# Kernel tuning notes

Measured on AMD Instinct MI355X. Metric: run time of the kernel, lower is better.

Reference implementation:

```python
import jax, jax.numpy as jnp
import numpy as np

C = 256        # channels per FPN level (in_channels == representation_size)
PATCH = 5      # GNN kernel_size == stride
NEG_SLOPE = 0.2
K = 7          # node_connectivities[0]


def _conv1x1(x, w, b):
    return jnp.einsum('bchw,oc->bohw', x, w) + b[None, :, None, None]


def _conv3x3(x, w, b):
    y = jax.lax.conv_general_dilated(x, w, (1, 1), 'SAME',
                                     dimension_numbers=('NCHW', 'OIHW', 'NCHW'))
    return y + b[None, :, None, None]


def _nearest(x, hout, wout):
    hin, win = x.shape[-2:]
    ih = (jnp.arange(hout) * hin) // hout
    iw = (jnp.arange(wout) * win) // wout
    return x[..., ih, :][..., iw]


def _topk_edges(score, k, n):
    # torch: A.scatter(1, topk_idx, topk_val); edge = nonzero(triu(A)); edge=[col,row]
    vals, idx = jax.lax.top_k(score, k)          # per-row top-k
    row = jnp.repeat(jnp.arange(n), k)
    col = idx.reshape(-1)
    val = vals.reshape(-1)
    # triu keeps col>=row; GATv2Conv removes self loops then re-adds one per node
    mask = (col > row) & (val != 0.0)
    loop = jnp.arange(n)
    src = jnp.concatenate([col, loop])           # PyG edge_index[0] = source
    dst = jnp.concatenate([row, loop])
    emask = jnp.concatenate([mask, jnp.ones((n,), bool)])
    return src, dst, emask


def _gatv2(x, src, dst, emask, wl, bl, wr, br, att, bias, n):
    heads, dout = att.shape
    xl = (x @ wl + bl).reshape(n, heads, dout)   # source transform (lin_l)
    xr = (x @ wr + br).reshape(n, heads, dout)   # target transform (lin_r)
    m = xl[src] + xr[dst]                        # [E, H, D]
    e = jnp.sum(jax.nn.leaky_relu(m, NEG_SLOPE) * att[None], axis=-1)  # [E, H]
    e = jnp.where(emask[:, None], e, -1e30)
    emax = jax.ops.segment_max(e, dst, num_segments=n)
    w = jnp.exp(e - emax[dst]) * emask[:, None]
    denom = jax.ops.segment_sum(w, dst, num_segments=n)
    alpha = w / (denom[dst] + 1e-16)
    out = jax.ops.segment_sum(alpha[..., None] * xl[src], dst, num_segments=n)
    return out.reshape(n, heads * dout) + bias


def _gnn(x, p, k):
    # x: [1, C, H, W], H,W divisible by PATCH
    _, c, hh, ww = x.shape
    nh, nw = hh // PATCH, ww // PATCH
    n = nh * nw
    patches = x[0].reshape(c, nh, PATCH, nw, PATCH).transpose(1, 3, 0, 2, 4)
    patches = patches.reshape(n, c, PATCH, PATCH)
    emb = jax.nn.relu(jnp.einsum('ncij,ocij->no', patches, p['conv1_w']) + p['conv1_b'])
    emb = jax.nn.relu(emb @ p['fc2_w'].T + p['fc2_b'])
    # feature-similarity kNN graph
    src, dst, em = _topk_edges(emb @ emb.T, k, n)
    h = jax.nn.elu(_gatv2(emb, src, dst, em, *p['g1'], n))
    h = jax.nn.elu(_gatv2(h, src, dst, em, *p['g2'], n))
    # spatial kNN graph (k smallest distances; self distance 0 drops out via val!=0)
    ii, jj = jnp.meshgrid(jnp.arange(nh) * PATCH, jnp.arange(nw) * PATCH, indexing='ij')
    centers = jnp.stack([ii.reshape(-1), jj.reshape(-1)], -1).astype(x.dtype)
    dist = jnp.sqrt(jnp.sum((centers[:, None] - centers[None]) ** 2, -1))
    src2, dst2, em2 = _topk_edges(-dist, k, n)
    h2 = jax.nn.elu(_gatv2(emb, src2, dst2, em2, *p['g3'], n))
    h2 = jax.nn.elu(_gatv2(h2, src2, dst2, em2, *p['g4'], n))
    hc = jax.nn.relu(jnp.concatenate([h, h2], 1) @ p['fc3_w'].T + p['fc3_b']) + h2
    # torch: reshape(dim,dim,C).swapdims(-1,0) -> [C, nw, nh]
    grid = jnp.transpose(hc.reshape(nh, nw, c), (2, 1, 0))
    # ConvTranspose2d(C, C, 5, stride=5): non-overlapping tiling
    up = jnp.einsum('cij,coab->oiajb', grid, p['convT_w'])
    up = up.reshape(c, nw * PATCH, nh * PATCH) + p['convT_b'][:, None, None]
    return jax.nn.relu(up)[None]


def _forward(feat0, feat1, inner_w, inner_b, layer_w, layer_b, convT_w, convT_b,
             conv1_w, conv1_b, fc2_w, fc2_b, fc3_w, fc3_b,
             g1_wl, g1_bl, g1_wr, g1_br, g1_att, g1_bias,
             g2_wl, g2_bl, g2_wr, g2_br, g2_att, g2_bias,
             g3_wl, g3_bl, g3_wr, g3_br, g3_att, g3_bias,
             g4_wl, g4_bl, g4_wr, g4_br, g4_att, g4_bias, k):
    feats = [feat0, feat1]
    xs = []
    for i, f in enumerate(feats):
        p = dict(conv1_w=conv1_w[i], conv1_b=conv1_b[i],
                 fc2_w=fc2_w[i], fc2_b=fc2_b[i],
                 fc3_w=fc3_w[i], fc3_b=fc3_b[i],
                 convT_w=convT_w[i], convT_b=convT_b[i],
                 g1=(g1_wl[i], g1_bl[i], g1_wr[i], g1_br[i], g1_att[i], g1_bias[i]),
                 g2=(g2_wl[i], g2_bl[i], g2_wr[i], g2_br[i], g2_att[i], g2_bias[i]),
                 g3=(g3_wl[i], g3_bl[i], g3_wr[i], g3_br[i], g3_att[i], g3_bias[i]),
                 g4=(g4_wl[i], g4_bl[i], g4_wr[i], g4_br[i], g4_att[i], g4_bias[i]))
        xs.append(f + _gnn(f, p, k))
    # top-down FPN
    last = _conv1x1(xs[1], inner_w[1], inner_b[1])
    out1 = _conv3x3(last, layer_w[1], layer_b[1])
    inner0 = _conv1x1(xs[0], inner_w[0], inner_b[0])
    td = _nearest(last, xs[0].shape[-2], xs[0].shape[-1])
    out0 = _conv3x3(inner0 + td, layer_w[0], layer_b[0])
    return out0, out1


def setup_inputs() -> dict:
    key = jax.random.key(0)
    keys = jax.random.split(key, 48)
    it = iter(range(48))
    def rn(shape, s=0.05):
        return (jax.random.normal(keys[next(it)], shape) * s).astype(jnp.float32)
    H8 = 8 * C
    inp = dict(
        feat0=rn((1, C, 200, 200), 1.0),
        feat1=rn((1, C, 100, 100), 1.0),
        inner_w=rn((2, C, C)), inner_b=rn((2, C)),
        layer_w=rn((2, C, C, 3, 3)), layer_b=rn((2, C)),
        convT_w=rn((2, C, C, PATCH, PATCH)), convT_b=rn((2, C)),
        conv1_w=rn((2, C, C, PATCH, PATCH)), conv1_b=rn((2, C)),
        fc2_w=rn((2, C, C)), fc2_b=rn((2, C)),
        fc3_w=rn((2, C, 2 * C)), fc3_b=rn((2, C)),
        g1_wl=rn((2, C, H8)), g1_bl=rn((2, H8)), g1_wr=rn((2, C, H8)), g1_br=rn((2, H8)),
        g1_att=rn((2, 8, C)), g1_bias=rn((2, H8)),
        g2_wl=rn((2, H8, C)), g2_bl=rn((2, C)), g2_wr=rn((2, H8, C)), g2_br=rn((2, C)),
        g2_att=rn((2, 1, C)), g2_bias=rn((2, C)),
        g3_wl=rn((2, C, H8)), g3_bl=rn((2, H8)), g3_wr=rn((2, C, H8)), g3_br=rn((2, H8)),
        g3_att=rn((2, 8, C)), g3_bias=rn((2, H8)),
        g4_wl=rn((2, H8, C)), g4_bl=rn((2, C)), g4_wr=rn((2, H8, C)), g4_br=rn((2, C)),
        g4_att=rn((2, 1, C)), g4_bias=rn((2, C)),
        k=K,
    )
    return inp


def reference(feat0, feat1, inner_w, inner_b, layer_w, layer_b, convT_w, convT_b,
              conv1_w, conv1_b, fc2_w, fc2_b, fc3_w, fc3_b,
              g1_wl, g1_bl, g1_wr, g1_br, g1_att, g1_bias,
              g2_wl, g2_bl, g2_wr, g2_br, g2_att, g2_bias,
              g3_wl, g3_bl, g3_wr, g3_br, g3_att, g3_bias,
              g4_wl, g4_bl, g4_wr, g4_br, g4_att, g4_bias, k):
    return _forward(feat0, feat1, inner_w, inner_b, layer_w, layer_b, convT_w, convT_b,
                    conv1_w, conv1_b, fc2_w, fc2_b, fc3_w, fc3_b,
                    g1_wl, g1_bl, g1_wr, g1_br, g1_att, g1_bias,
                    g2_wl, g2_bl, g2_wr, g2_br, g2_att, g2_bias,
                    g3_wl, g3_bl, g3_wr, g3_br, g3_att, g3_bias,
                    g4_wl, g4_bl, g4_wr, g4_br, g4_att, g4_bias, k)
```

## Files before the change

### kernel.cpp

```cpp
#include <hip/hip_runtime.h>
#include <cstdint>
#include <cstddef>
#include <math.h>

#define KNN 7

using short8  = __attribute__((ext_vector_type(8))) short;
using floatx4 = __attribute__((ext_vector_type(4))) float;

static const size_t OFF_ARENA = 0;
static const size_t OFF_XS0   = 10240000;
static const size_t OFF_XS1   = 20480000;
static const size_t OFF_LAST  = 23040000;
static const size_t OFF_EMB   = 25600000;
static const size_t OFF_EMB2  = 26009600;
static const size_t OFF_XL    = 26419200;
static const size_t OFF_H1    = 32972800;
static const size_t OFF_XL2   = 36249600;
static const size_t OFF_CAT   = 37068800;
static const size_t OFF_HC    = 37888000;
static const size_t OFF_SRCF  = 38400000;
static const size_t OFF_SRCS  = 38411200;
static const size_t OFF_BF_A  = 38422400;
static const size_t OFF_BF_W  = 40122400;

static __device__ __forceinline__ unsigned short f2bf(float f) {
    union { float f; unsigned u; } v; v.f = f;
    unsigned u = v.u;
    unsigned r = u + 0x7fffu + ((u >> 16) & 1u);
    return (unsigned short)(r >> 16);
}

static __device__ __forceinline__ void glds16(const void* g, void* l) {
    __builtin_amdgcn_global_load_lds((const __attribute__((address_space(1))) void*)g,
                                     (__attribute__((address_space(3))) void*)l, 16, 0, 0);
}

template<int ACT, bool BIAS>
__global__ __launch_bounds__(256)
void gemm_k(const float* __restrict__ A, const float* __restrict__ B,
            const float* __restrict__ bias, float* __restrict__ C, int M, int N, int K)
{
    __shared__ float As[16][68];
    __shared__ float Bs[16][68];
    const int tid = threadIdx.x;
    const int bm0 = blockIdx.y * 64;
    const int bn0 = blockIdx.x * 64;
    const int tx = tid & 15, ty = tid >> 4;
    const int lrow = tid >> 2;
    const int lk4  = (tid & 3) << 2;
    const int m = bm0 + lrow;
    const int nn = bn0 + lrow;
    const bool aok = m < M, bok = nn < N;
    float acc[4][4] = {{0.f,0.f,0.f,0.f},{0.f,0.f,0.f,0.f},{0.f,0.f,0.f,0.f},{0.f,0.f,0.f,0.f}};

    float4 va = {0.f,0.f,0.f,0.f}, vb = {0.f,0.f,0.f,0.f};
    if (aok) va = *(const float4*)(A + (size_t)m * K + lk4);
    if (bok) vb = *(const float4*)(B + (size_t)nn * K + lk4);

    for (int k0 = 0; k0 < K; k0 += 16) {
        As[lk4+0][lrow]=va.x; As[lk4+1][lrow]=va.y; As[lk4+2][lrow]=va.z; As[lk4+3][lrow]=va.w;
        Bs[lk4+0][lrow]=vb.x; Bs[lk4+1][lrow]=vb.y; Bs[lk4+2][lrow]=vb.z; Bs[lk4+3][lrow]=vb.w;
        __syncthreads();
        float4 na = {0.f,0.f,0.f,0.f}, nb = {0.f,0.f,0.f,0.f};
        const bool more = (k0 + 16) < K;
        if (more) {
            if (aok) na = *(const float4*)(A + (size_t)m * K + (k0 + 16 + lk4));
            if (bok) nb = *(const float4*)(B + (size_t)nn * K + (k0 + 16 + lk4));
        }
        #pragma unroll
        for (int k = 0; k < 16; k++) {
            const float4 av = *(const float4*)&As[k][ty << 2];
            const float4 bv = *(const float4*)&Bs[k][tx << 2];
            const float a0=av.x,a1=av.y,a2=av.z,a3=av.w;
            const float b0=bv.x,b1=bv.y,b2=bv.z,b3=bv.w;
            acc[0][0]=fmaf(a0,b0,acc[0][0]); acc[0][1]=fmaf(a0,b1,acc[0][1]);
            acc[0][2]=fmaf(a0,b2,acc[0][2]); acc[0][3]=fmaf(a0,b3,acc[0][3]);
            acc[1][0]=fmaf(a1,b0,acc[1][0]); acc[1][1]=fmaf(a1,b1,acc[1][1]);
            acc[1][2]=fmaf(a1,b2,acc[1][2]); acc[1][3]=fmaf(a1,b3,acc[1][3]);
            acc[2][0]=fmaf(a2,b0,acc[2][0]); acc[2][1]=fmaf(a2,b1,acc[2][1]);
            acc[2][2]=fmaf(a2,b2,acc[2][2]); acc[2][3]=fmaf(a2,b3,acc[2][3]);
            acc[3][0]=fmaf(a3,b0,acc[3][0]); acc[3][1]=fmaf(a3,b1,acc[3][1]);
            acc[3][2]=fmaf(a3,b2,acc[3][2]); acc[3][3]=fmaf(a3,b3,acc[3][3]);
        }
        __syncthreads();
        va = na; vb = nb;
    }
    #pragma unroll
    for (int i = 0; i < 4; i++) {
        const int mm = bm0 + (ty << 2) + i;
        if (mm >= M) continue;
        #pragma unroll
        for (int jj = 0; jj < 4; jj++) {
            const int nc = bn0 + (tx << 2) + jj;
            if (nc >= N) continue;
            float v = acc[i][jj];
            if (BIAS) v += bias[nc];
            if (ACT == 1) v = fmaxf(v, 0.f);
            C[(size_t)mm * N + nc] = v;
        }
    }
}

template<int ACT, bool BIAS>
static inline void gemm32(hipStream_t s, const float* A, const float* B, const float* bias,
                          float* C, int M, int N, int K)
{
    dim3 g((N + 63) / 64, (M + 63) / 64);
    gemm_k<ACT, BIAS><<<g, dim3(256), 0, s>>>(A, B, bias, C, M, N, K);
}

__global__ __launch_bounds__(256)
void gemm32_sk_k(const float* __restrict__ A, const float* __restrict__ B,
                 float* __restrict__ part, int M, int N, int K, int Kc)
{
    __shared__ float As[16][68];
    __shared__ float Bs[16][68];
    const int tid = threadIdx.x;
    const int bm0 = blockIdx.y * 64;
    const int bn0 = blockIdx.x * 64;
    const int sblk = blockIdx.z;
    const int kbeg = sblk * Kc;
    const int kend = (kbeg + Kc < K) ? kbeg + Kc : K;
    const int tx = tid & 15, ty = tid >> 4;
    const int lrow = tid >> 2;
    const int lk4  = (tid & 3) << 2;
    const int m = bm0 + lrow;
    const int nn = bn0 + lrow;
    const bool aok = m < M, bok = nn < N;
    float acc[4][4] = {{0.f,0.f,0.f,0.f},{0.f,0.f,0.f,0.f},{0.f,0.f,0.f,0.f},{0.f,0.f,0.f,0.f}};

    float4 va = {0.f,0.f,0.f,0.f}, vb = {0.f,0.f,0.f,0.f};
    if (aok) va = *(const float4*)(A + (size_t)m * K + kbeg + lk4);
    if (bok) vb = *(const float4*)(B + (size_t)nn * K + kbeg + lk4);

    for (int k0 = kbeg; k0 < kend; k0 += 16) {
        As[lk4+0][lrow]=va.x; As[lk4+1][lrow]=va.y; As[lk4+2][lrow]=va.z; As[lk4+3][lrow]=va.w;
        Bs[lk4+0][lrow]=vb.x; Bs[lk4+1][lrow]=vb.y; Bs[lk4+2][lrow]=vb.z; Bs[lk4+3][lrow]=vb.w;
        __syncthreads();
        float4 na = {0.f,0.f,0.f,0.f}, nb = {0.f,0.f,0.f,0.f};
        const bool more = (k0 + 16) < kend;
        if (more) {
            if (aok) na = *(const float4*)(A + (size_t)m * K + (k0 + 16 + lk4));
            if (bok) nb = *(const float4*)(B + (size_t)nn * K + (k0 + 16 + lk4));
        }
        #pragma unroll
        for (int k = 0; k < 16; k++) {
            const float4 av = *(const float4*)&As[k][ty << 2];
            const float4 bv = *(const float4*)&Bs[k][tx << 2];
            const float a0=av.x,a1=av.y,a2=av.z,a3=av.w;
            const float b0=bv.x,b1=bv.y,b2=bv.z,b3=bv.w;
            acc[0][0]=fmaf(a0,b0,acc[0][0]); acc[0][1]=fmaf(a0,b1,acc[0][1]);
            acc[0][2]=fmaf(a0,b2,acc[0][2]); acc[0][3]=fmaf(a0,b3,acc[0][3]);
            acc[1][0]=fmaf(a1,b0,acc[1][0]); acc[1][1]=fmaf(a1,b1,acc[1][1]);
            acc[1][2]=fmaf(a1,b2,acc[1][2]); acc[1][3]=fmaf(a1,b3,acc[1][3]);
            acc[2][0]=fmaf(a2,b0,acc[2][0]); acc[2][1]=fmaf(a2,b1,acc[2][1]);
            acc[2][2]=fmaf(a2,b2,acc[2][2]); acc[2][3]=fmaf(a2,b3,acc[2][3]);
            acc[3][0]=fmaf(a3,b0,acc[3][0]); acc[3][1]=fmaf(a3,b1,acc[3][1]);
            acc[3][2]=fmaf(a3,b2,acc[3][2]); acc[3][3]=fmaf(a3,b3,acc[3][3]);
        }
        __syncthreads();
        va = na; vb = nb;
    }
    float* P = part + (size_t)sblk * M * N;
    #pragma unroll
    for (int i = 0; i < 4; i++) {
        const int mm = bm0 + (ty << 2) + i;
        if (mm >= M) continue;
        #pragma unroll
        for (int jj = 0; jj < 4; jj++) {
            const int nc = bn0 + (tx << 2) + jj;
            if (nc >= N) continue;
            P[(size_t)mm * N + nc] = acc[i][jj];
        }
    }
}

template<int ACT, bool BIAS>
__global__ void sk_reduce_k(const float* __restrict__ part, const float* __restrict__ bias,
                            float* __restrict__ C, int MN, int N, int S)
{
    const int i4 = (blockIdx.x * 256 + threadIdx.x) * 4;
    if (i4 >= MN) return;
    float4 a = *(const float4*)(part + i4);
    for (int s = 1; s < S; s++) {
        const float4 b = *(const float4*)(part + (size_t)s * MN + i4);
        a.x += b.x; a.y += b.y; a.z += b.z; a.w += b.w;
    }
    if (BIAS) {
        const int n = i4 % N;
        a.x += bias[n]; a.y += bias[n + 1]; a.z += bias[n + 2]; a.w += bias[n + 3];
    }
    if (ACT == 1) {
        a.x = fmaxf(a.x, 0.f); a.y = fmaxf(a.y, 0.f);
        a.z = fmaxf(a.z, 0.f); a.w = fmaxf(a.w, 0.f);
    }
    *(float4*)(C + i4) = a;
}

template<int ACT, bool BIAS>
static inline void gemm32_sk(hipStream_t s, const float* A, const float* B, const float* bias,
                             float* C, float* part, int M, int N, int K, int S)
{
    const int Kc = ((K / S + 15) / 16) * 16;
    dim3 g((N + 63) / 64, (M + 63) / 64, S);
    gemm32_sk_k<<<g, dim3(256), 0, s>>>(A, B, part, M, N, K, Kc);
    const int MN = M * N;
    sk_reduce_k<ACT, BIAS><<<dim3((MN / 4 + 255) / 256), dim3(256), 0, s>>>(part, bias, C, MN, N, S);
}

enum { BT_NT = 0, BT_CONV2 = 2 };

template<int BT, int ACT, int BAX, bool ADDMAT>
__global__ __launch_bounds__(256)
void bgemm_k(const unsigned short* __restrict__ A, const unsigned short* __restrict__ B,
             const float* __restrict__ bias, const float* __restrict__ bias2, int nsplit,
             const float* __restrict__ Dmat, int Dld,
             float* __restrict__ C, int M, int N, int K, int imH, int imW)
{
    __shared__ unsigned short As[3][4096];
    __shared__ unsigned short Bs[3][4096];
    const int tid  = threadIdx.x;
    const int lane = tid & 63;
    const int wid  = tid >> 6;
    const int quad = lane >> 4;
    const int l15  = lane & 15;
    const int wy = wid >> 1, wx = wid & 1;

    int bxx = blockIdx.x, byy = blockIdx.y;
    if (gridDim.y == 2) {
        const int nbx = gridDim.x;
        const int nwg = nbx * 2;
        const int hw  = byy * nbx + bxx;
        const int q = nwg >> 3, r = nwg & 7;
        const int x8 = hw & 7, d = hw >> 3;
        const int lg = (x8 < r) ? x8 * (q + 1) + d : r * (q + 1) + (x8 - r) * q + d;
        byy = lg & 1; bxx = lg >> 1;
    }
    const int bm0 = byy * 128;
    const int bn0 = bxx * 128;

    floatx4 zero = {0.f, 0.f, 0.f, 0.f};
    floatx4 acc[4][4];
    #pragma unroll
    for (int i = 0; i < 4; i++)
        #pragma unroll
        for (int j = 0; j < 4; j++) acc[i][j] = zero;

    const int l4 = lane >> 2;
    const int swc = (((lane & 3) ^ ((lane >> 3) & 3)) << 3);
    const int r0 = wid * 32 + l4;
    const int r1 = r0 + 16;
    int am0 = bm0 + r0; if (am0 > M - 1) am0 = M - 1;
    int am1 = bm0 + r1; if (am1 > M - 1) am1 = M - 1;
    const unsigned short* aP0 = A + (size_t)am0 * K + swc;
    const unsigned short* aP1 = A + (size_t)am1 * K + swc;

    const unsigned short* bP0;
    const unsigned short* bP1;
    if (BT == BT_NT) {
        int bn0r = bn0 + r0; if (bn0r > N - 1) bn0r = N - 1;
        int bn1r = bn0 + r1; if (bn1r > N - 1) bn1r = N - 1;
        bP0 = B + (size_t)bn0r * K + swc;
        bP1 = B + (size_t)bn1r * K + swc;
    } else {
        const int W2 = imW + 2;
        int pp0 = bn0 + r0; if (pp0 > N - 1) pp0 = N - 1;
        int pp1 = bn0 + r1; if (pp1 > N - 1) pp1 = N - 1;
        const int py0 = pp0 / imW, px0 = pp0 - py0 * imW;
        const int py1 = pp1 / imW, px1 = pp1 - py1 * imW;
        bP0 = B + ((size_t)(py0 + 1) * W2 + px0 + 1) * 256 + swc;
        bP1 = B + ((size_t)(py1 + 1) * W2 + px1 + 1) * 256 + swc;
    }

    auto stage = [&](int buf, int t) {
        const int k0 = t << 5;
        glds16(aP0 + k0, &As[buf][wid * 1024]);
        glds16(aP1 + k0, &As[buf][wid * 1024 + 512]);
        if (BT == BT_NT) {
            glds16(bP0 + k0, &Bs[buf][wid * 1024]);
            glds16(bP1 + k0, &Bs[buf][wid * 1024 + 512]);
        } else {
            const int jj = k0 >> 8;
            const int j3 = jj / 3;
            const ptrdiff_t toff = (ptrdiff_t)((j3 - 1) * (imW + 2) + (jj - j3 * 3 - 1)) * 256
                                 + (k0 & 255);
            glds16(bP0 + toff, &Bs[buf][wid * 1024]);
            glds16(bP1 + toff, &Bs[buf][wid * 1024 + 512]);
        }
    };
    const int rsw = ((quad ^ ((l15 >> 1) & 3)) << 3);
    auto compute = [&](int buf) {
        short8 af[4], bfr[4];
        #pragma unroll
        for (int i = 0; i < 4; i++)
            af[i] = *(const short8*)&As[buf][(wy * 64 + i * 16 + l15) * 32 + rsw];
        #pragma unroll
        for (int j = 0; j < 4; j++)
            bfr[j] = *(const short8*)&Bs[buf][(wx * 64 + j * 16 + l15) * 32 + rsw];
        #pragma unroll
        for (int i = 0; i < 4; i++)
            #pragma unroll
            for (int j = 0; j < 4; j++)
                acc[i][j] = __builtin_amdgcn_mfma_f32_16x16x32_bf16(af[i], bfr[j], acc[i][j], 0, 0, 0);
    };

    const int T = K >> 5;
    stage(0, 0);
    if (T > 1) stage(1, 1);
    int cb = 0, sb = 2;
    for (int t = 0; t < T; t++) {
        if (t < T - 1) asm volatile("s_waitcnt vmcnt(4) lgkmcnt(0)" ::: "memory");
        else           asm volatile("s_waitcnt vmcnt(0) lgkmcnt(0)" ::: "memory");
        __builtin_amdgcn_s_barrier();
        __builtin_amdgcn_sched_barrier(0);
        if (t + 2 < T) stage(sb, t + 2);
        compute(cb);
        cb = (cb == 2) ? 0 : cb + 1;
        sb = (sb == 2) ? 0 : sb + 1;
    }

    #pragma unroll
    for (int i = 0; i < 4; i++) {
        #pragma unroll
        for (int r = 0; r < 4; r++) {
            const int m = bm0 + wy * 64 + i * 16 + quad * 4 + r;
            if (m >= M) continue;
            #pragma unroll
            for (int j = 0; j < 4; j++) {
                const int n = bn0 + wx * 64 + j * 16 + l15;
                if (n >= N) continue;
                float v = acc[i][j][r];
                if (bias != nullptr)
                    v += (BAX == 0) ? bias[m] : (n < nsplit ? bias[n] : bias2[n - nsplit]);
                if (ACT == 1) v = fmaxf(v, 0.f);
                if (ADDMAT) v += Dmat[(size_t)m * Dld + n];
                C[(size_t)m * N + n] = v;
            }
        }
    }
}

template<int BT, int ACT, int BAX, bool ADDMAT>
static inline void bgemm(hipStream_t s, const unsigned short* A, const unsigned short* B,
                         const float* bias, const float* bias2, int nsplit,
                         const float* D, int Dld, float* C,
                         int M, int N, int K, int imH = 0, int imW = 0)
{
    dim3 g((N + 127) / 128, (M + 127) / 128);
    bgemm_k<BT, ACT, BAX, ADDMAT><<<g, dim3(256), 0, s>>>(A, B, bias, bias2, nsplit,
                                                          D, Dld, C, M, N, K, imH, imW);
}

__global__ __launch_bounds__(256)
void bgemm_sk_k(const unsigned short* __restrict__ A, const unsigned short* __restrict__ B,
                float* __restrict__ part, int M, int N, int K, int Kc)
{
    __shared__ unsigned short As[3][4096];
    __shared__ unsigned short Bs[3][4096];
    const int tid  = threadIdx.x;
    const int lane = tid & 63;
    const int wid  = tid >> 6;
    const int quad = lane >> 4;
    const int l15  = lane & 15;
    const int wy = wid >> 1, wx = wid & 1;
    const int bm0 = blockIdx.y * 128;
    const int bn0 = blockIdx.x * 128;
    const int kbeg = blockIdx.z * Kc;
    const int kend = (kbeg + Kc < K) ? kbeg + Kc : K;

    floatx4 zero = {0.f, 0.f, 0.f, 0.f};
    floatx4 acc[4][4];
    #pragma unroll
    for (int i = 0; i < 4; i++)
        #pragma unroll
        for (int j = 0; j < 4; j++) acc[i][j] = zero;

    const int l4 = lane >> 2;
    const int swc = (((lane & 3) ^ ((lane >> 3) & 3)) << 3);
    const int r0 = wid * 32 + l4;
    const int r1 = r0 + 16;
    int am0 = bm0 + r0; if (am0 > M - 1) am0 = M - 1;
    int am1 = bm0 + r1; if (am1 > M - 1) am1 = M - 1;
    int bn0r = bn0 + r0; if (bn0r > N - 1) bn0r = N - 1;
    int bn1r = bn0 + r1; if (bn1r > N - 1) bn1r = N - 1;
    const unsigned short* aP0 = A + (size_t)am0 * K + kbeg + swc;
    const unsigned short* aP1 = A + (size_t)am1 * K + kbeg + swc;
    const unsigned short* bP0 = B + (size_t)bn0r * K + kbeg + swc;
    const unsigned short* bP1 = B + (size_t)bn1r * K + kbeg + swc;

    auto stage = [&](int buf, int t) {
        const int k0 = t << 5;
        glds16(aP0 + k0, &As[buf][wid * 1024]);
        glds16(aP1 + k0, &As[buf][wid * 1024 + 512]);
        glds16(bP0 + k0, &Bs[buf][wid * 1024]);
        glds16(bP1 + k0, &Bs[buf][wid * 1024 + 512]);
    };
    const int rsw = ((quad ^ ((l15 >> 1) & 3)) << 3);
    auto compute = [&](int buf) {
        short8 af[4], bfr[4];
        #pragma unroll
        for (int i = 0; i < 4; i++)
            af[i] = *(const short8*)&As[buf][(wy * 64 + i * 16 + l15) * 32 + rsw];
        #pragma unroll
        for (int j = 0; j < 4; j++)
            bfr[j] = *(const short8*)&Bs[buf][(wx * 64 + j * 16 + l15) * 32 + rsw];
        #pragma unroll
        for (int i = 0; i < 4; i++)
            #pragma unroll
            for (int j = 0; j < 4; j++)
                acc[i][j] = __builtin_amdgcn_mfma_f32_16x16x32_bf16(af[i], bfr[j], acc[i][j], 0, 0, 0);
    };

    const int T = (kend - kbeg) >> 5;
    stage(0, 0);
    if (T > 1) stage(1, 1);
    int cb = 0, sb = 2;
    for (int t = 0; t < T; t++) {
        if (t < T - 1) asm volatile("s_waitcnt vmcnt(4) lgkmcnt(0)" ::: "memory");
        else           asm volatile("s_waitcnt vmcnt(0) lgkmcnt(0)" ::: "memory");
        __builtin_amdgcn_s_barrier();
        __builtin_amdgcn_sched_barrier(0);
        if (t + 2 < T) stage(sb, t + 2);
        compute(cb);
        cb = (cb == 2) ? 0 : cb + 1;
        sb = (sb == 2) ? 0 : sb + 1;
    }

    float* P = part + (size_t)blockIdx.z * M * N;
    #pragma unroll
    for (int i = 0; i < 4; i++) {
        #pragma unroll
        for (int r = 0; r < 4; r++) {
            const int m = bm0 + wy * 64 + i * 16 + quad * 4 + r;
            if (m >= M) continue;
            #pragma unroll
            for (int j = 0; j < 4; j++) {
                const int n = bn0 + wx * 64 + j * 16 + l15;
                if (n >= N) continue;
                P[(size_t)m * N + n] = acc[i][j][r];
            }
        }
    }
}

template<int ACT, bool ADDMAT>
__global__ void bsk_reduce_k(const float* __restrict__ part,
                             const float* __restrict__ bias, const float* __restrict__ bias2,
                             int nsplit, const float* __restrict__ Dmat, int Dld,
                             float* __restrict__ C, int MN, int N, int S)
{
    const int i4 = (blockIdx.x * 256 + threadIdx.x) * 4;
    if (i4 >= MN) return;
    float4 a = *(const float4*)(part + i4);
    for (int s = 1; s < S; s++) {
        const float4 b = *(const float4*)(part + (size_t)s * MN + i4);
        a.x += b.x; a.y += b.y; a.z += b.z; a.w += b.w;
    }
    const int n = i4 % N;
    const float* bb = (n < nsplit) ? (bias + n) : (bias2 + n - nsplit);
    a.x += bb[0]; a.y += bb[1]; a.z += bb[2]; a.w += bb[3];
    if (ACT == 1) {
        a.x = fmaxf(a.x, 0.f); a.y = fmaxf(a.y, 0.f);
        a.z = fmaxf(a.z, 0.f); a.w = fmaxf(a.w, 0.f);
    }
    if (ADDMAT) {
        const int m = i4 / N;
        const float4 d = *(const float4*)(Dmat + (size_t)m * Dld + n);
        a.x += d.x; a.y += d.y; a.z += d.z; a.w += d.w;
    }
    *(float4*)(C + i4) = a;
}

template<int ACT, bool ADDMAT>
static inline void bgemm_sk(hipStream_t s, const unsigned short* A, const unsigned short* B,
                            const float* bias, const float* bias2, int nsplit,
                            const float* D, int Dld, float* C, float* part,
                            int M, int N, int K, int S)
{
    const int Kc = ((K / S + 31) / 32) * 32;
    dim3 g((N + 127) / 128, (M + 127) / 128, S);
    bgemm_sk_k<<<g, dim3(256), 0, s>>>(A, B, part, M, N, K, Kc);
    const int MN = M * N;
    bsk_reduce_k<ACT, ADDMAT><<<dim3((MN / 4 + 255) / 256), dim3(256), 0, s>>>(
        part, bias, bias2, nsplit, D, Dld, C, MN, N, S);
}

__global__ void cast_bf16_k(const float* __restrict__ in, unsigned short* __restrict__ out, int total)
{
    const int i4 = (blockIdx.x * 256 + threadIdx.x) * 4;
    if (i4 + 4 <= total) {
        const float4 v = *(const float4*)(in + i4);
        ushort4 o;
        o.x = f2bf(v.x); o.y = f2bf(v.y); o.z = f2bf(v.z); o.w = f2bf(v.w);
        *(ushort4*)(out + i4) = o;
    } else {
        for (int i = i4; i < total; i++) out[i] = f2bf(in[i]);
    }
}

static inline void cast_bf(hipStream_t s, const float* in, unsigned short* out, int total)
{
    cast_bf16_k<<<dim3((total / 4 + 255) / 256), dim3(256), 0, s>>>(in, out, total);
}

__device__ __forceinline__ void cast_t_body(const float* __restrict__ in,
                                            unsigned short* __restrict__ out, int K, int N)
{
    __shared__ float tile[64][65];
    const int n0 = blockIdx.x * 64;
    const int k0 = blockIdx.y * 64;
    const int t = threadIdx.x;
    const int r = t >> 2;
    const int c4 = (t & 3) << 4;
    {
        const int k = k0 + r;
        if (k < K && n0 + c4 + 16 <= N) {
            const float4* p = (const float4*)(in + (size_t)k * N + n0 + c4);
            *(float4*)&tile[r][c4]      = p[0];
            *(float4*)&tile[r][c4 + 4]  = p[1];
            *(float4*)&tile[r][c4 + 8]  = p[2];
            *(float4*)&tile[r][c4 + 12] = p[3];
        } else {
            for (int i = 0; i < 16; i++)
                tile[r][c4 + i] = (k < K && n0 + c4 + i < N) ? in[(size_t)k * N + n0 + c4 + i] : 0.f;
        }
    }
    __syncthreads();
    const int n = n0 + r;
    if (n >= N) return;
    unsigned short tmp[16];
    #pragma unroll
    for (int i = 0; i < 16; i++) tmp[i] = f2bf(tile[c4 + i][r]);
    if (k0 + 64 <= K) {
        *(uint4*)(out + (size_t)n * K + k0 + c4)     = *(uint4*)&tmp[0];
        *(uint4*)(out + (size_t)n * K + k0 + c4 + 8) = *(uint4*)&tmp[8];
    } else {
        for (int i = 0; i < 16; i++)
            if (k0 + c4 + i < K) out[(size_t)n * K + k0 + c4 + i] = tmp[i];
    }
}

__global__ void cast_t_k(const float* __restrict__ in, unsigned short* __restrict__ out, int K, int N)
{
    cast_t_body(in, out, K, N);
}

__global__ void cast_t2_k(const float* __restrict__ in0, const float* __restrict__ in1,
                          unsigned short* __restrict__ out0, unsigned short* __restrict__ out1,
                          int K, int N)
{
    if (blockIdx.z == 0) cast_t_body(in0, out0, K, N);
    else                 cast_t_body(in1, out1, K, N);
}

static inline void cast_t(hipStream_t s, const float* in, unsigned short* out, int K, int N)
{
    cast_t_k<<<dim3((N + 63) / 64, (K + 63) / 64), dim3(256), 0, s>>>(in, out, K, N);
}

static inline void cast_t2(hipStream_t s, const float* in0, const float* in1,
                           unsigned short* out0, unsigned short* out1, int K, int N)
{
    cast_t2_k<<<dim3((N + 63) / 64, (K + 63) / 64, 2), dim3(256), 0, s>>>(in0, in1, out0, out1, K, N);
}

__global__ void cast_t_pad_k(const float* __restrict__ in, unsigned short* __restrict__ out,
                             int N, int imW)
{
    __shared__ float tile[64][65];
    const int n0 = blockIdx.x * 64;
    const int k0 = blockIdx.y * 64;
    const int t = threadIdx.x;
    const int r = t >> 2;
    const int c4 = (t & 3) << 4;
    {
        const int k = k0 + r;
        if (n0 + c4 + 16 <= N) {
            const float4* p = (const float4*)(in + (size_t)k * N + n0 + c4);
            *(float4*)&tile[r][c4]      = p[0];
            *(float4*)&tile[r][c4 + 4]  = p[1];
            *(float4*)&tile[r][c4 + 8]  = p[2];
            *(float4*)&tile[r][c4 + 12] = p[3];
        } else {
            for (int i = 0; i < 16; i++)
                tile[r][c4 + i] = (n0 + c4 + i < N) ? in[(size_t)k * N + n0 + c4 + i] : 0.f;
        }
    }
    __syncthreads();
    const int n = n0 + r;
    if (n >= N) return;
    const int py = n / imW, px = n - py * imW;
    unsigned short tmp[16];
    #pragma unroll
    for (int i = 0; i < 16; i++) tmp[i] = f2bf(tile[c4 + i][r]);
    unsigned short* o = out + ((size_t)(py + 1) * (imW + 2) + px + 1) * 256 + k0 + c4;
    *(uint4*)(o)     = *(uint4*)&tmp[0];
    *(uint4*)(o + 8) = *(uint4*)&tmp[8];
}

static inline void cast_t_pad(hipStream_t s, const float* in, unsigned short* out, int N, int imW)
{
    cast_t_pad_k<<<dim3((N + 63) / 64, 4), dim3(256), 0, s>>>(in, out, N, imW);
}

__global__ void zero_ring_k(unsigned short* __restrict__ out, int imH, int imW)
{
    const int W2 = imW + 2;
    const int nb = 2 * W2 + 2 * imH;
    const int idx = blockIdx.x * 256 + threadIdx.x;
    if (idx >= nb * 32) return;
    const int p = idx >> 5;
    const int c8 = (idx & 31) << 3;
    int row;
    if (p < W2)            row = p;
    else if (p < 2 * W2)   row = (imH + 1) * W2 + (p - W2);
    else { const int q = p - 2 * W2; const int y = q >> 1;
           row = (y + 1) * W2 + ((q & 1) ? (imW + 1) : 0); }
    *(uint4*)(out + (size_t)row * 256 + c8) = (uint4){0, 0, 0, 0};
}

static inline void zero_ring(hipStream_t s, unsigned short* out, int imH, int imW)
{
    const int tot = (2 * (imW + 2) + 2 * imH) * 32;
    zero_ring_k<<<dim3((tot + 255) / 256), dim3(256), 0, s>>>(out, imH, imW);
}

__global__ void reorder_w3_k(const float* __restrict__ in, unsigned short* __restrict__ out)
{
    const int idx = blockIdx.x * 256 + threadIdx.x;
    if (idx >= 589824) return;
    const int o = idx / 2304;
    const int r = idx - o * 2304;
    const int j = r >> 8;
    const int c = r & 255;
    out[idx] = f2bf(in[(size_t)o * 2304 + c * 9 + j]);
}

__global__ void extract_patches_k(const float* __restrict__ f, float* __restrict__ patches,
                                  int nw, int H, int total)
{
    int idx = blockIdx.x * 256 + threadIdx.x;
    if (idx >= total) return;
    int q = idx % 6400;
    int p = idx / 6400;
    int c = q / 25;
    int rem = q - c * 25;
    int a = rem / 5, b = rem - (rem / 5) * 5;
    int ih = p / nw, iw = p - (p / nw) * nw;
    patches[idx] = f[(size_t)c * H * H + (size_t)(ih * 5 + a) * H + (iw * 5 + b)];
}

__global__ void topk_feat_k(const float* __restrict__ score, int* __restrict__ srcCols, int n)
{
    const int r = blockIdx.x;
    const int lane = threadIdx.x;
    const float* row = score + (size_t)r * n;
    int   sel[KNN];
    float selv[KNN];
    #pragma unroll
    for (int t = 0; t < KNN; t++) {
        float best = -__builtin_huge_valf();
        int   bidx = 0x7fffffff;
        for (int c = lane; c < n; c += 64) {
            bool taken = false;
            #pragma unroll
            for (int u = 0; u < KNN; u++)
                if (u < t && sel[u] == c) taken = true;
            if (taken) continue;
            float v = row[c];
            if (v > best || (v == best && c < bidx)) { best = v; bidx = c; }
        }
        #pragma unroll
        for (int off = 32; off > 0; off >>= 1) {
            float ov = __shfl_down(best, off);
            int   oi = __shfl_down(bidx, off);
            if (ov > best || (ov == best && oi < bidx)) { best = ov; bidx = oi; }
        }
        best = __shfl(best, 0);
        bidx = __shfl(bidx, 0);
        sel[t] = bidx; selv[t] = best;
    }
    if (lane < KNN) {
        int c = -1; float v = 0.f;
        #pragma unroll
        for (int t = 0; t < KNN; t++)
            if (lane == t) { c = sel[t]; v = selv[t]; }
        srcCols[r * KNN + lane] = (c > r && v != 0.0f) ? c : -1;
    }
}

__global__ void topk_spatial_k(int* __restrict__ srcCols, int n, int nw)
{
    const int r = blockIdx.x;
    const int lane = threadIdx.x;
    const int ri = r / nw, rj = r - (r / nw) * nw;
    int sel[KNN];
    #pragma unroll
    for (int t = 0; t < KNN; t++) {
        int bkey = 0x7fffffff;
        for (int c = lane; c < n; c += 64) {
            bool taken = false;
            #pragma unroll
            for (int u = 0; u < KNN; u++)
                if (u < t && sel[u] == c) taken = true;
            if (taken) continue;
            const int ci = c / nw, cj = c - (c / nw) * nw;
            const int dy = (ri - ci) * 5, dx = (rj - cj) * 5;
            const int d2 = dy * dy + dx * dx;
            const int key = (d2 << 11) | c;
            if (key < bkey) bkey = key;
        }
        #pragma unroll
        for (int off = 32; off > 0; off >>= 1) {
            int ok = __shfl_down(bkey, off);
            if (ok < bkey) bkey = ok;
        }
        bkey = __shfl(bkey, 0);
        sel[t] = bkey & 2047;
    }
    if (lane < KNN) {
        int c = -1;
        #pragma unroll
        for (int t = 0; t < KNN; t++) if (lane == t) c = sel[t];
        srcCols[r * KNN + lane] = (c > r) ? c : -1;
    }
}

__global__ void gat_fused_k(const float* __restrict__ x, int xroff, int xstride,
                            const float* __restrict__ att,
                            const int* __restrict__ srcCols, const float* __restrict__ bias,
                            float* __restrict__ out, int n, int H, int ostride, int ooff)
{
    const int wid = (blockIdx.x * blockDim.x + threadIdx.x) >> 6;
    const int lane = threadIdx.x & 63;
    if (wid >= n * H) return;
    const int h = wid % H;
    const int r = wid / H;
    const int d0 = lane << 2;

    const float4 xrf  = *(const float4*)(x + (size_t)r * xstride + xroff + h * 256 + d0);
    const float4 attf = *(const float4*)(att + (size_t)h * 256 + d0);

    int srcs[8];
    #pragma unroll
    for (int s_ = 0; s_ < KNN; s_++) srcs[s_] = srcCols[r * KNN + s_];
    srcs[7] = r;

    float4 xlf[8];
    float  e[8];
    #pragma unroll
    for (int s_ = 0; s_ < 8; s_++) {
        const int c = srcs[s_];
        float4 v = {0.f, 0.f, 0.f, 0.f};
        if (c >= 0) v = *(const float4*)(x + (size_t)c * xstride + h * 256 + d0);
        xlf[s_] = v;
        float m, p = 0.f;
        m = v.x + xrf.x; m = (m > 0.f) ? m : 0.2f * m; p += m * attf.x;
        m = v.y + xrf.y; m = (m > 0.f) ? m : 0.2f * m; p += m * attf.y;
        m = v.z + xrf.z; m = (m > 0.f) ? m : 0.2f * m; p += m * attf.z;
        m = v.w + xrf.w; m = (m > 0.f) ? m : 0.2f * m; p += m * attf.w;
        #pragma unroll
        for (int off = 32; off > 0; off >>= 1) p += __shfl_down(p, off);
        e[s_] = __shfl(p, 0);
    }

    float mx = e[7];
    #pragma unroll
    for (int s_ = 0; s_ < KNN; s_++)
        if (srcs[s_] >= 0) mx = fmaxf(mx, e[s_]);
    float a[8], denom = 0.f;
    #pragma unroll
    for (int s_ = 0; s_ < 8; s_++) {
        a[s_] = (s_ == 7 || srcs[s_] >= 0) ? expf(e[s_] - mx) : 0.f;
        denom += a[s_];
    }
    const float inv = 1.f / (denom + 1e-16f);

    float o0 = 0.f, o1 = 0.f, o2 = 0.f, o3 = 0.f;
    #pragma unroll
    for (int s_ = 0; s_ < 8; s_++) {
        const float al = a[s_] * inv;
        o0 = fmaf(al, xlf[s_].x, o0); o1 = fmaf(al, xlf[s_].y, o1);
        o2 = fmaf(al, xlf[s_].z, o2); o3 = fmaf(al, xlf[s_].w, o3);
    }
    const float* bb = bias + (size_t)h * 256 + d0;
    o0 += bb[0]; o1 += bb[1]; o2 += bb[2]; o3 += bb[3];
    o0 = (o0 > 0.f) ? o0 : (expf(o0) - 1.f);
    o1 = (o1 > 0.f) ? o1 : (expf(o1) - 1.f);
    o2 = (o2 > 0.f) ? o2 : (expf(o2) - 1.f);
    o3 = (o3 > 0.f) ? o3 : (expf(o3) - 1.f);
    float4 res = {o0, o1, o2, o3};
    *(float4*)(out + (size_t)r * ostride + ooff + (size_t)h * 256 + d0) = res;
}

__global__ void scatter_convT_k(const float* __restrict__ f, const float* __restrict__ U,
                                const float* __restrict__ bias, float* __restrict__ xs,
                                int nw, int H, int total)
{
    int idx = blockIdx.x * 256 + threadIdx.x;
    if (idx >= total) return;
    int x = idx % H;
    int t = idx / H;
    int y = t % H;
    int o = t / H;
    int j = y / 5, a = y - j * 5;
    int i = x / 5, b = x - i * 5;
    int p = i * nw + j;
    float v = U[(size_t)p * 6400 + o * 25 + a * 5 + b] + bias[o];
    v = fmaxf(v, 0.f);
    xs[idx] = f[idx] + v;
}

__global__ void upsample_add_k(float* __restrict__ acc, const float* __restrict__ last,
                               int H, int Hs, int total)
{
    int idx = blockIdx.x * 256 + threadIdx.x;
    if (idx >= total) return;
    int x = idx % H;
    int t = idx / H;
    int y = t % H;
    int c = t / H;
    acc[idx] += last[(size_t)c * Hs * Hs + (size_t)(y >> 1) * Hs + (x >> 1)];
}

static void run_level(void* const* d_in, float* ws, int l, int H, hipStream_t s)
{
    const float* f = (const float*)d_in[l];
    const int nh = H / 5, nw = nh, n = nh * nw, HW = H * H;

    const float* convT_w = (const float*)d_in[6]  + (size_t)l * 1638400;
    const float* convT_b = (const float*)d_in[7]  + l * 256;
    const float* conv1_w = (const float*)d_in[8]  + (size_t)l * 1638400;
    const float* conv1_b = (const float*)d_in[9]  + l * 256;
    const float* fc2_w   = (const float*)d_in[10] + (size_t)l * 65536;
    const float* fc2_b   = (const float*)d_in[11] + l * 256;
    const float* fc3_w   = (const float*)d_in[12] + (size_t)l * 131072;
    const float* fc3_b   = (const float*)d_in[13] + l * 256;
    const float* g1_wl   = (const float*)d_in[14] + (size_t)l * 524288;
    const float* g1_bl   = (const float*)d_in[15] + l * 2048;
    const float* g1_wr   = (const float*)d_in[16] + (size_t)l * 524288;
    const float* g1_br   = (const float*)d_in[17] + l * 2048;
    const float* g1_att  = (const float*)d_in[18] + l * 2048;
    const float* g1_bias = (const float*)d_in[19] + l * 2048;
    const float* g2_wl   = (const float*)d_in[20] + (size_t)l * 524288;
    const float* g2_bl   = (const float*)d_in[21] + l * 256;
    const float* g2_wr   = (const float*)d_in[22] + (size_t)l * 524288;
    const float* g2_br   = (const float*)d_in[23] + l * 256;
    const float* g2_att  = (const float*)d_in[24] + l * 256;
    const float* g2_bias = (const float*)d_in[25] + l * 256;
    const float* g3_wl   = (const float*)d_in[26] + (size_t)l * 524288;
    const float* g3_bl   = (const float*)d_in[27] + l * 2048;
    const float* g3_wr   = (const float*)d_in[28] + (size_t)l * 524288;
    const float* g3_br   = (const float*)d_in[29] + l * 2048;
    const float* g3_att  = (const float*)d_in[30] + l * 2048;
    const float* g3_bias = (const float*)d_in[31] + l * 2048;
    const float* g4_wl   = (const float*)d_in[32] + (size_t)l * 524288;
    const float* g4_bl   = (const float*)d_in[33] + l * 256;
    const float* g4_wr   = (const float*)d_in[34] + (size_t)l * 524288;
    const float* g4_br   = (const float*)d_in[35] + l * 256;
    const float* g4_att  = (const float*)d_in[36] + l * 256;
    const float* g4_bias = (const float*)d_in[37] + l * 256;

    float* patches = ws + OFF_ARENA;
    float* xs    = ws + (l == 0 ? OFF_XS0 : OFF_XS1);
    float* emb   = ws + OFF_EMB;
    float* emb2  = ws + OFF_EMB2;
    float* score = ws + OFF_LAST;
    float* xlr   = ws + OFF_XL;
    float* h1    = ws + OFF_H1;
    float* xlr2  = ws + OFF_XL2;
    float* cat   = ws + OFF_CAT;
    float* hc    = ws + OFF_HC;
    int* srcF = (int*)(ws + OFF_SRCF);
    int* srcS = (int*)(ws + OFF_SRCS);
    unsigned short* ba = (unsigned short*)(ws + OFF_BF_A);
    unsigned short* bw = (unsigned short*)(ws + OFF_BF_W);
    float* part = ws + OFF_ARENA;

    { int tot = n * 6400;
      extract_patches_k<<<dim3((tot + 255) / 256), dim3(256), 0, s>>>(f, patches, nw, H, tot); }

    gemm32_sk<1, true>(s, patches, conv1_w, conv1_b, emb, xlr, n, 256, 6400, 16);
    gemm32<1, true>(s, emb, fc2_w, fc2_b, emb2, n, 256, 256);
    gemm32<0, false>(s, emb2, emb2, nullptr, score, n, n, 256);
    topk_feat_k<<<dim3(n), dim3(64), 0, s>>>(score, srcF, n);
    topk_spatial_k<<<dim3(n), dim3(64), 0, s>>>(srcS, n, nw);

    const int gatw1 = n * 8;
    const int gatw2 = n;

    cast_bf(s, emb2, ba, n * 256);
    cast_t2(s, g1_wl, g1_wr, bw, bw + 2048 * 256, 256, 2048);
    if (n >= 1024)
        bgemm<BT_NT, 0, 1, false>(s, ba, bw, g1_bl, g1_br, 2048, nullptr, 0, xlr, n, 4096, 256);
    else
        bgemm_sk<0, false>(s, ba, bw, g1_bl, g1_br, 2048, nullptr, 0, xlr, part, n, 4096, 256, 2);
    gat_fused_k<<<dim3((gatw1 + 3) / 4), dim3(256), 0, s>>>(xlr, 2048, 4096, g1_att, srcF, g1_bias, h1, n, 8, 2048, 0);

    cast_bf(s, h1, ba, n * 2048);
    cast_t2(s, g2_wl, g2_wr, bw, bw + 256 * 2048, 2048, 256);
    bgemm_sk<0, false>(s, ba, bw, g2_bl, g2_br, 256, nullptr, 0, xlr2, part, n, 512, 2048, 8);
    gat_fused_k<<<dim3((gatw2 + 3) / 4), dim3(256), 0, s>>>(xlr2, 256, 512, g2_att, srcF, g2_bias, cat, n, 1, 512, 0);

    cast_bf(s, emb2, ba, n * 256);
    cast_t2(s, g3_wl, g3_wr, bw, bw + 2048 * 256, 256, 2048);
    if (n >= 1024)
        bgemm<BT_NT, 0, 1, false>(s, ba, bw, g3_bl, g3_br, 2048, nullptr, 0, xlr, n, 4096, 256);
    else
        bgemm_sk<0, false>(s, ba, bw, g3_bl, g3_br, 2048, nullptr, 0, xlr, part, n, 4096, 256, 2);
    gat_fused_k<<<dim3((gatw1 + 3) / 4), dim3(256), 0, s>>>(xlr, 2048, 4096, g3_att, srcS, g3_bias, h1, n, 8, 2048, 0);

    cast_bf(s, h1, ba, n * 2048);
    cast_t2(s, g4_wl, g4_wr, bw, bw + 256 * 2048, 2048, 256);
    bgemm_sk<0, false>(s, ba, bw, g4_bl, g4_br, 256, nullptr, 0, xlr2, part, n, 512, 2048, 8);
    gat_fused_k<<<dim3((gatw2 + 3) / 4), dim3(256), 0, s>>>(xlr2, 256, 512, g4_att, srcS, g4_bias, cat, n, 1, 512, 256);

    cast_bf(s, cat, ba, n * 512);
    cast_bf(s, fc3_w, bw, 131072);
    bgemm_sk<1, true>(s, ba, bw, fc3_b, fc3_b, 256, cat + 256, 512, hc, part, n, 256, 512, 4);
    cast_bf(s, hc, ba, n * 256);
    cast_t(s, convT_w, bw, 256, 6400);
    bgemm<BT_NT, 0, 1, false>(s, ba, bw, nullptr, nullptr, 0, nullptr, 0, patches, n, 6400, 256);
    { int tot = 256 * HW;
      scatter_convT_k<<<dim3((tot + 255) / 256), dim3(256), 0, s>>>(f, patches, convT_b, xs, nw, H, tot); }
}

extern "C" void kernel_launch(void* const* d_in, const int* in_sizes, int n_in,
                              void* d_out, int out_size, void* d_ws, size_t ws_size,
                              hipStream_t stream)
{
    float* ws  = (float*)d_ws;
    float* out = (float*)d_out;

    run_level(d_in, ws, 0, 200, stream);
    run_level(d_in, ws, 1, 100, stream);

    const float* inner_w = (const float*)d_in[2];
    const float* inner_b = (const float*)d_in[3];
    const float* layer_w = (const float*)d_in[4];
    const float* layer_b = (const float*)d_in[5];
    float* xs0    = ws + OFF_XS0;
    float* xs1    = ws + OFF_XS1;
    float* last   = ws + OFF_LAST;
    float* inner0 = ws + OFF_ARENA;
    unsigned short* bimg = (unsigned short*)(ws + OFF_XL);
    unsigned short* bw1  = (unsigned short*)(ws + OFF_BF_W);
    unsigned short* bwc  = (unsigned short*)(ws + OFF_BF_W + 100000);

    cast_t(stream, xs1, bimg, 256, 10000);
    cast_bf(stream, inner_w + 65536, bw1, 65536);
    bgemm<BT_NT, 0, 0, false>(stream, bw1, bimg, inner_b + 256, nullptr, 0, nullptr, 0,
                              last, 256, 10000, 256);
    reorder_w3_k<<<dim3((589824 + 255) / 256), dim3(256), 0, stream>>>(layer_w + 589824, bwc);
    zero_ring(stream, bimg, 100, 100);
    cast_t_pad(stream, last, bimg, 10000, 100);
    bgemm<BT_CONV2, 0, 0, false>(stream, bwc, bimg, layer_b + 256, nullptr, 0, nullptr, 0,
                                 out + 10240000, 256, 10000, 2304, 100, 100);

    cast_t(stream, xs0, bimg, 256, 40000);
    cast_bf(stream, inner_w, bw1, 65536);
    bgemm<BT_NT, 0, 0, false>(stream, bw1, bimg, inner_b, nullptr, 0, nullptr, 0,
                              inner0, 256, 40000, 256);
    { int tot = 256 * 40000;
      upsample_add_k<<<dim3((tot + 255) / 256), dim3(256), 0, stream>>>(inner0, last, 200, 100, tot); }
    reorder_w3_k<<<dim3((589824 + 255) / 256), dim3(256), 0, stream>>>(layer_w, bwc);
    zero_ring(stream, bimg, 200, 200);
    cast_t_pad(stream, inner0, bimg, 40000, 200);
    bgemm<BT_CONV2, 0, 0, false>(stream, bwc, bimg, layer_b, nullptr, 0, nullptr, 0,
                                 out, 256, 40000, 2304, 200, 200);
}
```

Measured before the change: 1.156 ms.

## Replace fp32 split-K patch GEMM with bf16 hi/lo split MFMA GEMM

The patch-embedding GEMM (n x 6400 x 256) previously ran on an fp32 SIMT split-K kernel. It now splits the patches and conv weights into bf16 hi and lo parts and runs three MFMA products (hi*hi, lo*hi, hi*lo), with the K dimension split into slabs. The partial results are summed in the existing reduce kernel, which also adds bias and ReLU. This moves the dominant FLOPs onto the matrix cores while keeping close to fp32 accuracy, at the cost of extra cast passes, a weight split on every call, and a larger partial buffer to reduce.

New measurement: 1.116 ms. 1.04x faster.

```diff
diff --git a/kernel.cpp b/kernel.cpp
--- a/kernel.cpp
+++ b/kernel.cpp
@@ -31,6 +31,10 @@
     return (unsigned short)(r >> 16);
 }
 
+static __device__ __forceinline__ float bf2f(unsigned short h) {
+    union { unsigned u; float f; } v; v.u = ((unsigned)h) << 16; return v.f;
+}
+
 static __device__ __forceinline__ void glds16(const void* g, void* l) {
     __builtin_amdgcn_global_load_lds((const __attribute__((address_space(1))) void*)g,
                                      (__attribute__((address_space(3))) void*)l, 16, 0, 0);
@@ -108,105 +112,6 @@
 {
     dim3 g((N + 63) / 64, (M + 63) / 64);
     gemm_k<ACT, BIAS><<<g, dim3(256), 0, s>>>(A, B, bias, C, M, N, K);
-}
-
-__global__ __launch_bounds__(256)
-void gemm32_sk_k(const float* __restrict__ A, const float* __restrict__ B,
-                 float* __restrict__ part, int M, int N, int K, int Kc)
-{
-    __shared__ float As[16][68];
-    __shared__ float Bs[16][68];
-    const int tid = threadIdx.x;
-    const int bm0 = blockIdx.y * 64;
-    const int bn0 = blockIdx.x * 64;
-    const int sblk = blockIdx.z;
-    const int kbeg = sblk * Kc;
-    const int kend = (kbeg + Kc < K) ? kbeg + Kc : K;
-    const int tx = tid & 15, ty = tid >> 4;
-    const int lrow = tid >> 2;
-    const int lk4  = (tid & 3) << 2;
-    const int m = bm0 + lrow;
-    const int nn = bn0 + lrow;
-    const bool aok = m < M, bok = nn < N;
-    float acc[4][4] = {{0.f,0.f,0.f,0.f},{0.f,0.f,0.f,0.f},{0.f,0.f,0.f,0.f},{0.f,0.f,0.f,0.f}};
-
-    float4 va = {0.f,0.f,0.f,0.f}, vb = {0.f,0.f,0.f,0.f};
-    if (aok) va = *(const float4*)(A + (size_t)m * K + kbeg + lk4);
-    if (bok) vb = *(const float4*)(B + (size_t)nn * K + kbeg + lk4);
-
-    for (int k0 = kbeg; k0 < kend; k0 += 16) {
-        As[lk4+0][lrow]=va.x; As[lk4+1][lrow]=va.y; As[lk4+2][lrow]=va.z; As[lk4+3][lrow]=va.w;
-        Bs[lk4+0][lrow]=vb.x; Bs[lk4+1][lrow]=vb.y; Bs[lk4+2][lrow]=vb.z; Bs[lk4+3][lrow]=vb.w;
-        __syncthreads();
-        float4 na = {0.f,0.f,0.f,0.f}, nb = {0.f,0.f,0.f,0.f};
-        const bool more = (k0 + 16) < kend;
-        if (more) {
-            if (aok) na = *(const float4*)(A + (size_t)m * K + (k0 + 16 + lk4));
-            if (bok) nb = *(const float4*)(B + (size_t)nn * K + (k0 + 16 + lk4));
-        }
-        #pragma unroll
-        for (int k = 0; k < 16; k++) {
-            const float4 av = *(const float4*)&As[k][ty << 2];
-            const float4 bv = *(const float4*)&Bs[k][tx << 2];
-            const float a0=av.x,a1=av.y,a2=av.z,a3=av.w;
-            const float b0=bv.x,b1=bv.y,b2=bv.z,b3=bv.w;
-            acc[0][0]=fmaf(a0,b0,acc[0][0]); acc[0][1]=fmaf(a0,b1,acc[0][1]);
-            acc[0][2]=fmaf(a0,b2,acc[0][2]); acc[0][3]=fmaf(a0,b3,acc[0][3]);
-            acc[1][0]=fmaf(a1,b0,acc[1][0]); acc[1][1]=fmaf(a1,b1,acc[1][1]);
-            acc[1][2]=fmaf(a1,b2,acc[1][2]); acc[1][3]=fmaf(a1,b3,acc[1][3]);
-            acc[2][0]=fmaf(a2,b0,acc[2][0]); acc[2][1]=fmaf(a2,b1,acc[2][1]);
-            acc[2][2]=fmaf(a2,b2,acc[2][2]); acc[2][3]=fmaf(a2,b3,acc[2][3]);
-            acc[3][0]=fmaf(a3,b0,acc[3][0]); acc[3][1]=fmaf(a3,b1,acc[3][1]);
-            acc[3][2]=fmaf(a3,b2,acc[3][2]); acc[3][3]=fmaf(a3,b3,acc[3][3]);
-        }
-        __syncthreads();
-        va = na; vb = nb;
-    }
-    float* P = part + (size_t)sblk * M * N;
-    #pragma unroll
-    for (int i = 0; i < 4; i++) {
-        const int mm = bm0 + (ty << 2) + i;
-        if (mm >= M) continue;
-        #pragma unroll
-        for (int jj = 0; jj < 4; jj++) {
-            const int nc = bn0 + (tx << 2) + jj;
-            if (nc >= N) continue;
-            P[(size_t)mm * N + nc] = acc[i][jj];
-        }
-    }
-}
-
-template<int ACT, bool BIAS>
-__global__ void sk_reduce_k(const float* __restrict__ part, const float* __restrict__ bias,
-                            float* __restrict__ C, int MN, int N, int S)
-{
-    const int i4 = (blockIdx.x * 256 + threadIdx.x) * 4;
-    if (i4 >= MN) return;
-    float4 a = *(const float4*)(part + i4);
-    for (int s = 1; s < S; s++) {
-        const float4 b = *(const float4*)(part + (size_t)s * MN + i4);
-        a.x += b.x; a.y += b.y; a.z += b.z; a.w += b.w;
-    }
-    if (BIAS) {
-        const int n = i4 % N;
-        a.x += bias[n]; a.y += bias[n + 1]; a.z += bias[n + 2]; a.w += bias[n + 3];
-    }
-    if (ACT == 1) {
-        a.x = fmaxf(a.x, 0.f); a.y = fmaxf(a.y, 0.f);
-        a.z = fmaxf(a.z, 0.f); a.w = fmaxf(a.w, 0.f);
-    }
-    *(float4*)(C + i4) = a;
-}
-
-template<int ACT, bool BIAS>
-static inline void gemm32_sk(hipStream_t s, const float* A, const float* B, const float* bias,
-                             float* C, float* part, int M, int N, int K, int S)
-{
-    const int Kc = ((K / S + 15) / 16) * 16;
-    dim3 g((N + 63) / 64, (M + 63) / 64, S);
-    gemm32_sk_k<<<g, dim3(256), 0, s>>>(A, B, part, M, N, K, Kc);
-    const int MN = M * N;
-    sk_reduce_k<ACT, BIAS><<<dim3((MN / 4 + 255) / 256), dim3(256), 0, s>>>(part, bias, C, MN, N, S);
 }
 
 enum { BT_NT = 0, BT_CONV2 = 2 };
@@ -444,6 +349,104 @@
     }
 }
 
+__global__ __launch_bounds__(256)
+void bgemm_hilo_sk_k(const unsigned short* __restrict__ Ahi, const unsigned short* __restrict__ Alo,
+                     const unsigned short* __restrict__ Bhi, const unsigned short* __restrict__ Blo,
+                     float* __restrict__ part, int M, int N, int K, int Kc, int S3)
+{
+    __shared__ unsigned short As[3][4096];
+    __shared__ unsigned short Bs[3][4096];
+    const int tid  = threadIdx.x;
+    const int lane = tid & 63;
+    const int wid  = tid >> 6;
+    const int quad = lane >> 4;
+    const int l15  = lane & 15;
+    const int wy = wid >> 1, wx = wid & 1;
+    const int bm0 = blockIdx.y * 128;
+    const int bn0 = blockIdx.x * 128;
+
+    const int seg  = blockIdx.z / S3;
+    const int slab = blockIdx.z - seg * S3;
+    const unsigned short* A = (seg == 1) ? Alo : Ahi;
+    const unsigned short* B = (seg == 2) ? Blo : Bhi;
+    const int kbeg = slab * Kc;
+    const int kend = (kbeg + Kc < K) ? kbeg + Kc : K;
+
+    floatx4 zero = {0.f, 0.f, 0.f, 0.f};
+    floatx4 acc[4][4];
+    #pragma unroll
+    for (int i = 0; i < 4; i++)
+        #pragma unroll
+        for (int j = 0; j < 4; j++) acc[i][j] = zero;
+
+    const int l4 = lane >> 2;
+    const int swc = (((lane & 3) ^ ((lane >> 3) & 3)) << 3);
+    const int r0 = wid * 32 + l4;
+    const int r1 = r0 + 16;
+    int am0 = bm0 + r0; if (am0 > M - 1) am0 = M - 1;
+    int am1 = bm0 + r1; if (am1 > M - 1) am1 = M - 1;
+    int bn0r = bn0 + r0; if (bn0r > N - 1) bn0r = N - 1;
+    int bn1r = bn0 + r1; if (bn1r > N - 1) bn1r = N - 1;
+    const unsigned short* aP0 = A + (size_t)am0 * K + kbeg + swc;
+    const unsigned short* aP1 = A + (size_t)am1 * K + kbeg + swc;
+    const unsigned short* bP0 = B + (size_t)bn0r * K + kbeg + swc;
+    const unsigned short* bP1 = B + (size_t)bn1r * K + kbeg + swc;
+
+    auto stage = [&](int buf, int t) {
+        const int k0 = t << 5;
+        glds16(aP0 + k0, &As[buf][wid * 1024]);
+        glds16(aP1 + k0, &As[buf][wid * 1024 + 512]);
+        glds16(bP0 + k0, &Bs[buf][wid * 1024]);
+        glds16(bP1 + k0, &Bs[buf][wid * 1024 + 512]);
+    };
+    const int rsw = ((quad ^ ((l15 >> 1) & 3)) << 3);
+    auto compute = [&](int buf) {
+        short8 af[4], bfr[4];
+        #pragma unroll
+        for (int i = 0; i < 4; i++)
+            af[i] = *(const short8*)&As[buf][(wy * 64 + i * 16 + l15) * 32 + rsw];
+        #pragma unroll
+        for (int j = 0; j < 4; j++)
+            bfr[j] = *(const short8*)&Bs[buf][(wx * 64 + j * 16 + l15) * 32 + rsw];
+        #pragma unroll
+        for (int i = 0; i < 4; i++)
+            #pragma unroll
+            for (int j = 0; j < 4; j++)
+                acc[i][j] = __builtin_amdgcn_mfma_f32_16x16x32_bf16(af[i], bfr[j], acc[i][j], 0, 0, 0);
+    };
+
+    const int T = (kend - kbeg) >> 5;
+    stage(0, 0);
+    if (T > 1) stage(1, 1);
+    int cb = 0, sb = 2;
+    for (int t = 0; t < T; t++) {
+        if (t < T - 1) asm volatile("s_waitcnt vmcnt(4) lgkmcnt(0)" ::: "memory");
+        else           asm volatile("s_waitcnt vmcnt(0) lgkmcnt(0)" ::: "memory");
+        __builtin_amdgcn_s_barrier();
+        __builtin_amdgcn_sched_barrier(0);
+        if (t + 2 < T) stage(sb, t + 2);
+        compute(cb);
+        cb = (cb == 2) ? 0 : cb + 1;
+        sb = (sb == 2) ? 0 : sb + 1;
+    }
+
+    float* P = part + (size_t)blockIdx.z * M * N;
+    #pragma unroll
+    for (int i = 0; i < 4; i++) {
+        #pragma unroll
+        for (int r = 0; r < 4; r++) {
+            const int m = bm0 + wy * 64 + i * 16 + quad * 4 + r;
+            if (m >= M) continue;
+            #pragma unroll
+            for (int j = 0; j < 4; j++) {
+                const int n = bn0 + wx * 64 + j * 16 + l15;
+                if (n >= N) continue;
+                P[(size_t)m * N + n] = acc[i][j][r];
+            }
+        }
+    }
+}
+
 template<int ACT, bool ADDMAT>
 __global__ void bsk_reduce_k(const float* __restrict__ part,
                              const float* __restrict__ bias, const float* __restrict__ bias2,
@@ -502,6 +505,27 @@
 static inline void cast_bf(hipStream_t s, const float* in, unsigned short* out, int total)
 {
     cast_bf16_k<<<dim3((total / 4 + 255) / 256), dim3(256), 0, s>>>(in, out, total);
+}
+
+__global__ void cast_hilo_k(const float* __restrict__ in, unsigned short* __restrict__ hi,
+                            unsigned short* __restrict__ lo, int total)
+{
+    const int i4 = (blockIdx.x * 256 + threadIdx.x) * 4;
+    if (i4 + 4 <= total) {
+        const float4 v = *(const float4*)(in + i4);
+        ushort4 h, l;
+        h.x = f2bf(v.x); l.x = f2bf(v.x - bf2f(h.x));
+        h.y = f2bf(v.y); l.y = f2bf(v.y - bf2f(h.y));
+        h.z = f2bf(v.z); l.z = f2bf(v.z - bf2f(h.z));
+        h.w = f2bf(v.w); l.w = f2bf(v.w - bf2f(h.w));
+        *(ushort4*)(hi + i4) = h;
+        *(ushort4*)(lo + i4) = l;
+    } else {
+        for (int i = i4; i < total; i++) {
+            unsigned short h = f2bf(in[i]);
+            hi[i] = h; lo[i] = f2bf(in[i] - bf2f(h));
+        }
+    }
 }
 
 __device__ __forceinline__ void cast_t_body(const float* __restrict__ in,
@@ -637,8 +661,10 @@
     out[idx] = f2bf(in[(size_t)o * 2304 + c * 9 + j]);
 }
 
-__global__ void extract_patches_k(const float* __restrict__ f, float* __restrict__ patches,
-                                  int nw, int H, int total)
+__global__ void extract_patches_hilo_k(const float* __restrict__ f,
+                                       unsigned short* __restrict__ hi,
+                                       unsigned short* __restrict__ lo,
+                                       int nw, int H, int total)
 {
     int idx = blockIdx.x * 256 + threadIdx.x;
     if (idx >= total) return;
@@ -648,7 +674,10 @@
     int rem = q - c * 25;
     int a = rem / 5, b = rem - (rem / 5) * 5;
     int ih = p / nw, iw = p - (p / nw) * nw;
-    patches[idx] = f[(size_t)c * H * H + (size_t)(ih * 5 + a) * H + (iw * 5 + b)];
+    const float v = f[(size_t)c * H * H + (size_t)(ih * 5 + a) * H + (iw * 5 + b)];
+    const unsigned short h = f2bf(v);
+    hi[idx] = h;
+    lo[idx] = f2bf(v - bf2f(h));
 }
 
 __global__ void topk_feat_k(const float* __restrict__ score, int* __restrict__ srcCols, int n)
@@ -878,10 +907,20 @@
     unsigned short* bw = (unsigned short*)(ws + OFF_BF_W);
     float* part = ws + OFF_ARENA;
 
+    unsigned short* Ahi = (unsigned short*)(ws + OFF_ARENA);
+    unsigned short* Alo = Ahi + (size_t)n * 6400;
+    unsigned short* Whi = (unsigned short*)(ws + OFF_BF_A);
+    unsigned short* Wlo = Whi + 1638400;
     { int tot = n * 6400;
-      extract_patches_k<<<dim3((tot + 255) / 256), dim3(256), 0, s>>>(f, patches, nw, H, tot); }
-
-    gemm32_sk<1, true>(s, patches, conv1_w, conv1_b, emb, xlr, n, 256, 6400, 16);
+      extract_patches_hilo_k<<<dim3((tot + 255) / 256), dim3(256), 0, s>>>(f, Ahi, Alo, nw, H, tot); }
+    cast_hilo_k<<<dim3((1638400 / 4 + 255) / 256), dim3(256), 0, s>>>(conv1_w, Whi, Wlo, 1638400);
+    const int S3 = (l == 0) ? 4 : 8;
+    { dim3 g(2, (n + 127) / 128, 3 * S3);
+      bgemm_hilo_sk_k<<<g, dim3(256), 0, s>>>(Ahi, Alo, Whi, Wlo, xlr, n, 256, 6400, 6400 / S3, S3); }
+    { const int MN = n * 256;
+      bsk_reduce_k<1, false><<<dim3((MN / 4 + 255) / 256), dim3(256), 0, s>>>(
+          xlr, conv1_b, conv1_b, 256, nullptr, 0, emb, MN, 256, 3 * S3); }
+
     gemm32<1, true>(s, emb, fc2_w, fc2_b, emb2, n, 256, 256);
     gemm32<0, false>(s, emb2, emb2, nullptr, score, n, n, 256);
     topk_feat_k<<<dim3(n), dim3(64), 0, s>>>(score, srcF, n);
```
